# Performance work log

Hardware: AMD Instinct MI355X
Metric: run time of the kernel (lower is better)

Reference implementation:

```python
import jax, jax.numpy as jnp
import numpy as np

NT, NTR, NQ = 2048, 4096, 257  # time samples, traces, quantile knots


def cumtrapz(y, dx):
    # cumulative trapezoid along last axis, zero-prepended (preserve_dims=True)
    c = jnp.cumsum((y[..., 1:] + y[..., :-1]) * (0.5 * dx), axis=-1)
    return jnp.concatenate([jnp.zeros_like(y[..., :1]), c], axis=-1)


def trapz(y, dx):
    return (jnp.sum(y, axis=-1) - 0.5 * (y[..., 0] + y[..., -1])) * dx


def renorm(f, dx):
    # square + normalize to a pdf along time (standard W2-FWI renormalization)
    g = f * f
    return g / trapz(g, dx)[..., None]


def true_quantile(pdf, x, p, dx):
    # step-function quantile: invert clipped CDF via searchsorted per trace
    cdf = jnp.clip(cumtrapz(pdf, dx), 0.0, 1.0)  # [B, nt]
    idx = jax.vmap(lambda c: jnp.searchsorted(c, p))(cdf)  # [B, nq]
    idx = jnp.clip(idx, 0, x.shape[0] - 1)
    return x[idx]  # [B, nq]


def natural_cubic_coeffs(p, q):
    # batched natural cubic spline of q(p); knots p shared across batch
    h = p[1:] - p[:-1]                                 # [n-1]
    slope = (q[..., 1:] - q[..., :-1]) / h             # [B, n-1]
    rhs = 6.0 * (slope[..., 1:] - slope[..., :-1])     # [B, n-2]
    diag = 2.0 * (h[:-1] + h[1:])
    off = h[1:-1]
    T = jnp.diag(diag) + jnp.diag(off, 1) + jnp.diag(off, -1)  # [n-2, n-2], shared
    M_inner = jnp.linalg.solve(T, rhs[..., None])[..., 0]      # [B, n-2]
    z = jnp.zeros_like(q[..., :1])
    M = jnp.concatenate([z, M_inner, z], axis=-1)      # natural BCs: M0 = Mn = 0
    a = q[..., :-1]
    b = slope - h * (2.0 * M[..., :-1] + M[..., 1:]) / 6.0
    c = 0.5 * M[..., :-1]
    d = (M[..., 1:] - M[..., :-1]) / (6.0 * h)
    return a, b, c, d  # each [B, n-1]


def spline_eval(p, a, b, c, d, tq):
    # vectorized batched spline evaluation (replaces per-element Python loop)
    idx = jnp.clip(jnp.searchsorted(p, tq, side='left') - 1, 0, p.shape[0] - 2)
    frac = tq - p[idx]
    ga = jnp.take_along_axis(a, idx, axis=-1)
    gb = jnp.take_along_axis(b, idx, axis=-1)
    gc = jnp.take_along_axis(c, idx, axis=-1)
    gd = jnp.take_along_axis(d, idx, axis=-1)
    return ga + frac * (gb + frac * (gc + frac * gd))


def w2_forward(f, obs_data, t, p):
    dx = t[1] - t[0]
    # constructor-time part: quantile splines of observed data
    q = true_quantile(renorm(obs_data, dx), t, p, dx)   # [B, nq]
    a, b, c, d = natural_cubic_coeffs(p, q)
    # forward: CDF of synthetic, composed with observed quantile
    F = cumtrapz(renorm(f, dx), dx)                     # [B, nt]
    off_diag = spline_eval(p, a, b, c, d, F)            # [B, nt]
    diff = (t[None, :] - off_diag) ** 2
    integrated = trapz(diff * f, dx)                    # [B]
    return jnp.sum(integrated)


def setup_inputs() -> dict:
    key = jax.random.key(0)
    k1, k2 = jax.random.split(key)
    f = jax.random.normal(k1, (NTR, NT), dtype=jnp.float32)
    obs_data = jax.random.normal(k2, (NTR, NT), dtype=jnp.float32)
    t = jnp.linspace(0.0, 2.0, NT, dtype=jnp.float32)
    p = jnp.linspace(0.0, 1.0, NQ, dtype=jnp.float32)
    return {"f": f, "obs_data": obs_data, "t": t, "p": p}


def reference(f, obs_data, t, p):
    return w2_forward(f, obs_data, t, p)
```

## Files before the change

### kernel.cpp

```cpp
#include <hip/hip_runtime.h>

#define TPB 256
#define NT_ 2048
#define NQ_ 257
#define EPT 8
#define BWQ 5
#define BWS (BWQ + 2)
#define BD2 (2*BWQ + 3)
#define PQ BWQ
#define QLEN (PQ + NQ_ + BWQ + 2)
#define H_P 0.00390625f
#define RTPB 1024

struct Band { float v[BD2 * 256]; };
constexpr Band make_band() {
  Band b{};
  double L[256] = {}, winv[256] = {};
  const double H = 1.0 / 256.0;
  winv[0] = 1.0 / (4.0 * H);
  L[0] = 0.0;
  for (int i = 1; i < 255; i++) {
    L[i] = H * winv[i - 1];
    winv[i] = 1.0 / (4.0 * H - L[i] * H);
  }
  for (int i = 0; i < 255; i++) {
    double col[2 * BWS + 1] = {};
    double y[BWS + 1] = {};
    y[0] = 1.0;
    for (int m = 1; m <= BWS; m++) {
      int idx = i + m;
      y[m] = (idx <= 254) ? (-L[idx] * y[m - 1]) : 0.0;
    }
    double xn = 0.0;
    for (int m = BWS; m >= 0; m--) {
      int idx = i + m;
      double val = 0.0;
      if (idx <= 254) {
        double num = y[m] - ((idx < 254) ? H * xn : 0.0);
        val = num * winv[idx];
        xn = val;
      }
      col[m + BWS] = val;
    }
    for (int m = -1; m >= -BWS; m--) {
      int idx = i + m;
      double val = 0.0;
      if (idx >= 0) {
        val = (-H * xn) * winv[idx];
        xn = val;
      }
      col[m + BWS] = val;
    }
    for (int mm = 0; mm < BD2; mm++) {
      int n = i - BWQ + mm;
      double w = 0.0;
      if (n >= 0 && n <= 256) {
        double s0 = 0.0, s1 = 0.0, s2 = 0.0;
        int d0 = n - i, d1 = n - 1 - i, d2 = n - 2 - i;
        if (n     >= 0 && n     <= 254 && d0 >= -BWS && d0 <= BWS) s0 = col[d0 + BWS];
        if (n - 1 >= 0 && n - 1 <= 254 && d1 >= -BWS && d1 <= BWS) s1 = col[d1 + BWS];
        if (n - 2 >= 0 && n - 2 <= 254 && d2 >= -BWS && d2 <= BWS) s2 = col[d2 + BWS];
        w = 1536.0 * (s0 - 2.0 * s1 + s2);
      }
      b.v[mm * 256 + i] = (float)w;
    }
  }
  return b;
}
__device__ __constant__ Band g_band = make_band();

__device__ __forceinline__ double shfl_down_f64(double x, int off) {
  union { double d; int i[2]; } u; u.d = x;
  u.i[0] = __shfl_down(u.i[0], off, 64);
  u.i[1] = __shfl_down(u.i[1], off, 64);
  return u.d;
}

template<int CTRL, int RM, int BM, bool BC>
__device__ __forceinline__ float dppf(float x) {
  return __int_as_float(__builtin_amdgcn_update_dpp(
      0, __float_as_int(x), CTRL, RM, BM, BC));
}
template<int CTRL, int RM, int BM, bool BC>
__device__ __forceinline__ double dppd(double x) {
  union { double d; int i[2]; } u, o; u.d = x;
  o.i[0] = __builtin_amdgcn_update_dpp(0, u.i[0], CTRL, RM, BM, BC);
  o.i[1] = __builtin_amdgcn_update_dpp(0, u.i[1], CTRL, RM, BM, BC);
  return o.d;
}
__device__ __forceinline__ void iscan2(float& a, float& b) {
  a += dppf<0x111,0xF,0xF,true >(a);  b += dppf<0x111,0xF,0xF,true >(b);
  a += dppf<0x112,0xF,0xF,true >(a);  b += dppf<0x112,0xF,0xF,true >(b);
  a += dppf<0x114,0xF,0xF,true >(a);  b += dppf<0x114,0xF,0xF,true >(b);
  a += dppf<0x118,0xF,0xF,true >(a);  b += dppf<0x118,0xF,0xF,true >(b);
  a += dppf<0x142,0xa,0xF,false>(a);  b += dppf<0x142,0xa,0xF,false>(b);
  a += dppf<0x143,0xc,0xF,false>(a);  b += dppf<0x143,0xc,0xF,false>(b);
}
__device__ __forceinline__ void iscan2d(double& a, double& b) {
  a += dppd<0x111,0xF,0xF,true >(a);  b += dppd<0x111,0xF,0xF,true >(b);
  a += dppd<0x112,0xF,0xF,true >(a);  b += dppd<0x112,0xF,0xF,true >(b);
  a += dppd<0x114,0xF,0xF,true >(a);  b += dppd<0x114,0xF,0xF,true >(b);
  a += dppd<0x118,0xF,0xF,true >(a);  b += dppd<0x118,0xF,0xF,true >(b);
  a += dppd<0x142,0xa,0xF,false>(a);  b += dppd<0x142,0xa,0xF,false>(b);
  a += dppd<0x143,0xc,0xF,false>(a);  b += dppd<0x143,0xc,0xF,false>(b);
}

__global__ __launch_bounds__(TPB) void w2_main(
    const float* __restrict__ f, const float* __restrict__ obs,
    const float* __restrict__ t, double* __restrict__ row_out) {
  __shared__ float s_qA[QLEN], s_qB[QLEN];
  __shared__ float4 s_coefA[256], s_coefB[256];
  __shared__ float s_wfA[4], s_wfB[4], s_wf2A[4], s_wf2B[4];
  __shared__ double s_wdA[4], s_wdB[4];
  __shared__ double s_miscA[2], s_miscB[2];

  const int tid = threadIdx.x;
  const int lane = tid & 63;
  const int wid = tid >> 6;
  const int rowA = (int)blockIdx.x * 2;
  const int rowB = rowA + 1;
  const int base = tid * EPT;
  const int emax = (tid == TPB - 1) ? EPT - 1 : EPT;

  const double dx = (double)t[1] - (double)t[0];

  if (tid < PQ) { s_qA[tid] = 0.0f; s_qB[tid] = 0.0f; }
  if (tid >= TPB - (BWQ + 2)) {
    int o = PQ + NQ_ + tid - (TPB - (BWQ + 2));
    s_qA[o] = 0.0f; s_qB[o] = 0.0f;
  }

  float tl[EPT + 1];
  {
    const float4 a = *reinterpret_cast<const float4*>(t + base);
    const float4 b = *reinterpret_cast<const float4*>(t + base + 4);
    tl[0] = a.x; tl[1] = a.y; tl[2] = a.z; tl[3] = a.w;
    tl[4] = b.x; tl[5] = b.y; tl[6] = b.z; tl[7] = b.w;
  }
  tl[EPT] = (tid < TPB - 1) ? t[base + EPT] : 0.0f;

  float sAA[EPT], sAB[EPT];
  float epA = 0.0f, epB = 0.0f;
  {
    const float* orA = obs + (size_t)rowA * NT_;
    const float* orB = obs + (size_t)rowB * NT_;
    float ovA[EPT + 1], ovB[EPT + 1];
    {
      const float4 a0 = *reinterpret_cast<const float4*>(orA + base);
      const float4 a1 = *reinterpret_cast<const float4*>(orA + base + 4);
      const float4 b0 = *reinterpret_cast<const float4*>(orB + base);
      const float4 b1 = *reinterpret_cast<const float4*>(orB + base + 4);
      ovA[0] = a0.x; ovA[1] = a0.y; ovA[2] = a0.z; ovA[3] = a0.w;
      ovA[4] = a1.x; ovA[5] = a1.y; ovA[6] = a1.z; ovA[7] = a1.w;
      ovB[0] = b0.x; ovB[1] = b0.y; ovB[2] = b0.z; ovB[3] = b0.w;
      ovB[4] = b1.x; ovB[5] = b1.y; ovB[6] = b1.z; ovB[7] = b1.w;
    }
    ovA[EPT] = (tid < TPB - 1) ? orA[base + EPT] : 0.0f;
    ovB[EPT] = (tid < TPB - 1) ? orB[base + EPT] : 0.0f;
    for (int k = 0; k < emax; k++) {
      sAA[k] = ovA[k] * ovA[k] + ovA[k + 1] * ovA[k + 1];
      sAB[k] = ovB[k] * ovB[k] + ovB[k + 1] * ovB[k + 1];
      epA += sAA[k];
      epB += sAB[k];
    }
    if (emax < EPT) { sAA[EPT - 1] = 0.0f; sAB[EPT - 1] = 0.0f; }
  }
  float vA = epA, vB = epB;
  iscan2(vA, vB);
  float exclA = __shfl_up(vA, 1, 64);
  float exclB = __shfl_up(vB, 1, 64);
  if (lane == 0) { exclA = 0.0f; exclB = 0.0f; }
  if (lane == 63) { s_wfA[wid] = vA; s_wfB[wid] = vB; }
  __syncthreads();
  float woffA = 0.0f, totA = 0.0f, woffB = 0.0f, totB = 0.0f;
  #pragma unroll
  for (int w = 0; w < 4; w++) {
    float swA = s_wfA[w], swB = s_wfB[w];
    if (w < wid) { woffA += swA; woffB += swB; }
    totA += swA; totB += swB;
  }
  float runA = woffA + exclA, inclA = woffA + vA;
  float runB = woffB + exclB, inclB = woffB + vB;
  float invA256 = 256.0f / totA;
  float invB256 = 256.0f / totB;

  {
    float cprevS = fminf(runA * invA256, 256.0f);
    int j = (int)cprevS + 1;
    float r = runA;
    for (int k = 0; k < emax; k++) {
      float cu_uns = (k == emax - 1) ? inclA : (r + sAA[k]);
      r = cu_uns;
      float cuS = fminf(cu_uns * invA256, 256.0f);
      int jh = (int)cuS;
      float tq = tl[k + 1];
      for (; j <= jh; j++) s_qA[PQ + j] = tq;
    }
    if (tid == 0) s_qA[PQ + 0] = tl[0];
    if (tid == TPB - 1) {
      float tq = tl[EPT - 1];
      for (; j <= 256; j++) s_qA[PQ + j] = tq;
    }
  }
  {
    float cprevS = fminf(runB * invB256, 256.0f);
    int j = (int)cprevS + 1;
    float r = runB;
    for (int k = 0; k < emax; k++) {
      float cu_uns = (k == emax - 1) ? inclB : (r + sAB[k]);
      r = cu_uns;
      float cuS = fminf(cu_uns * invB256, 256.0f);
      int jh = (int)cuS;
      float tq = tl[k + 1];
      for (; j <= jh; j++) s_qB[PQ + j] = tq;
    }
    if (tid == 0) s_qB[PQ + 0] = tl[0];
    if (tid == TPB - 1) {
      float tq = tl[EPT - 1];
      for (; j <= 256; j++) s_qB[PQ + j] = tq;
    }
  }

  const float* frA = f + (size_t)rowA * NT_;
  const float* frB = f + (size_t)rowB * NT_;
  float fvA[EPT + 1], fvB[EPT + 1];
  {
    const float4 a0 = *reinterpret_cast<const float4*>(frA + base);
    const float4 a1 = *reinterpret_cast<const float4*>(frA + base + 4);
    const float4 b0 = *reinterpret_cast<const float4*>(frB + base);
    const float4 b1 = *reinterpret_cast<const float4*>(frB + base + 4);
    fvA[0] = a0.x; fvA[1] = a0.y; fvA[2] = a0.z; fvA[3] = a0.w;
    fvA[4] = a1.x; fvA[5] = a1.y; fvA[6] = a1.z; fvA[7] = a1.w;
    fvB[0] = b0.x; fvB[1] = b0.y; fvB[2] = b0.z; fvB[3] = b0.w;
    fvB[4] = b1.x; fvB[5] = b1.y; fvB[6] = b1.z; fvB[7] = b1.w;
  }
  fvA[EPT] = (tid < TPB - 1) ? frA[base + EPT] : 0.0f;
  fvB[EPT] = (tid < TPB - 1) ? frB[base + EPT] : 0.0f;

  float sBA[EPT], sBB[EPT];
  float ep2A = 0.0f, ep2B = 0.0f;
  for (int k = 0; k < emax; k++) {
    sBA[k] = fvA[k] * fvA[k] + fvA[k + 1] * fvA[k + 1];
    sBB[k] = fvB[k] * fvB[k] + fvB[k + 1] * fvB[k + 1];
    ep2A += sBA[k];
    ep2B += sBB[k];
  }
  if (emax < EPT) { sBA[EPT - 1] = 0.0f; sBB[EPT - 1] = 0.0f; }
  float v2A = ep2A, v2B = ep2B;
  iscan2(v2A, v2B);
  float excl2A = __shfl_up(v2A, 1, 64);
  float excl2B = __shfl_up(v2B, 1, 64);
  if (lane == 0) { excl2A = 0.0f; excl2B = 0.0f; }
  if (lane == 63) { s_wf2A[wid] = v2A; s_wf2B[wid] = v2B; }
  __syncthreads();

  float woff2A = 0.0f, tot2A = 0.0f, woff2B = 0.0f, tot2B = 0.0f;
  #pragma unroll
  for (int w = 0; w < 4; w++) {
    float swA = s_wf2A[w], swB = s_wf2B[w];
    if (w < wid) { woff2A += swA; woff2B += swB; }
    tot2A += swA; tot2B += swB;
  }
  float run2A = woff2A + excl2A, inv2A256 = 256.0f / tot2A;
  float run2B = woff2B + excl2B, inv2B256 = 256.0f / tot2B;

  float MregA = 0.0f, MregB = 0.0f;
  if (tid < 255) {
    #pragma unroll
    for (int mm = 0; mm < BD2; mm++) {
      float w = g_band.v[mm * 256 + tid];
      MregA += w * s_qA[tid + mm];
      MregB += w * s_qB[tid + mm];
    }
  }
  float MprevA = __shfl_up(MregA, 1, 64);
  float MprevB = __shfl_up(MregB, 1, 64);
  if (lane == 63) { s_wfA[wid] = MregA; s_wfB[wid] = MregB; }
  __syncthreads();
  if (lane == 0) {
    MprevA = (wid == 0) ? 0.0f : s_wfA[wid - 1];
    MprevB = (wid == 0) ? 0.0f : s_wfB[wid - 1];
  }

  {
    const float h = H_P;
    float q0A = s_qA[PQ + tid], q1A = s_qA[PQ + tid + 1];
    float slA = (q1A - q0A) * 256.0f;
    float bA = slA - h * (2.0f * MprevA + MregA) * (1.0f / 6.0f);
    float cA = 0.5f * MprevA;
    float dA = (MregA - MprevA) * (256.0f / 6.0f);
    s_coefA[tid] = make_float4(q0A, bA * (1.0f / 256.0f),
                               cA * (1.0f / 65536.0f), dA * (1.0f / 16777216.0f));
    float q0B = s_qB[PQ + tid], q1B = s_qB[PQ + tid + 1];
    float slB = (q1B - q0B) * 256.0f;
    float bB = slB - h * (2.0f * MprevB + MregB) * (1.0f / 6.0f);
    float cB = 0.5f * MprevB;
    float dB = (MregB - MprevB) * (256.0f / 6.0f);
    s_coefB[tid] = make_float4(q0B, bB * (1.0f / 256.0f),
                               cB * (1.0f / 65536.0f), dB * (1.0f / 16777216.0f));
  }
  __syncthreads();

  float csumA = 0.0f, csumB = 0.0f;
  {
    float r2A = run2A, r2B = run2B;
    #pragma unroll
    for (int k = 0; k < EPT; k++) {
      if (k > 0) { r2A += sBA[k - 1]; r2B += sBB[k - 1]; }
      float GA = r2A * inv2A256;
      float GB = r2B * inv2B256;
      float fiA = ceilf(GA) - 1.0f;
      float fiB = ceilf(GB) - 1.0f;
      fiA = fminf(fmaxf(fiA, 0.0f), 255.0f);
      fiB = fminf(fmaxf(fiB, 0.0f), 255.0f);
      int idxA = (int)fiA;
      int idxB = (int)fiB;
      float uA = GA - fiA;
      float uB = GB - fiB;
      float4 cfA = s_coefA[idxA];
      float4 cfB = s_coefB[idxB];
      float valA = cfA.x + uA * (cfA.y + uA * (cfA.z + uA * cfA.w));
      float valB = cfB.x + uB * (cfB.y + uB * (cfB.z + uB * cfB.w));
      float diffA = tl[k] - valA;
      float diffB = tl[k] - valB;
      float wvA = diffA * diffA * fvA[k];
      float wvB = diffB * diffB * fvB[k];
      if (tid == 0 && k == 0) { s_miscA[0] = (double)wvA; s_miscB[0] = (double)wvB; }
      if (tid == TPB - 1 && k == EPT - 1) { s_miscA[1] = (double)wvA; s_miscB[1] = (double)wvB; }
      csumA += wvA;
      csumB += wvB;
    }
  }
  double rA = (double)csumA, rB = (double)csumB;
  iscan2d(rA, rB);
  if (lane == 63) { s_wdA[wid] = rA; s_wdB[wid] = rB; }
  __syncthreads();
  if (tid == 0) {
    double totwA = s_wdA[0] + s_wdA[1] + s_wdA[2] + s_wdA[3];
    double totwB = s_wdB[0] + s_wdB[1] + s_wdB[2] + s_wdB[3];
    row_out[rowA] = (totwA - 0.5 * (s_miscA[0] + s_miscA[1])) * dx;
    row_out[rowB] = (totwB - 0.5 * (s_miscB[0] + s_miscB[1])) * dx;
  }
}

__global__ __launch_bounds__(RTPB) void w2_reduce(const double* __restrict__ row_out,
                                                  int ntr, float* __restrict__ out) {
  __shared__ double s[RTPB / 64];
  int tid = threadIdx.x, lane = tid & 63, wid = tid >> 6;
  double v = 0.0;
  for (int i = tid; i < ntr; i += RTPB) v += row_out[i];
  #pragma unroll
  for (int off = 32; off >= 1; off >>= 1) v += shfl_down_f64(v, off);
  if (lane == 0) s[wid] = v;
  __syncthreads();
  if (tid == 0) {
    double tot = 0.0;
    #pragma unroll
    for (int i = 0; i < RTPB / 64; i++) tot += s[i];
    out[0] = (float)tot;
  }
}

extern "C" void kernel_launch(void* const* d_in, const int* in_sizes, int n_in,
                              void* d_out, int out_size, void* d_ws, size_t ws_size,
                              hipStream_t stream) {
  const float* f   = (const float*)d_in[0];
  const float* obs = (const float*)d_in[1];
  const float* t   = (const float*)d_in[2];
  int nt = in_sizes[2];
  int ntr = in_sizes[0] / nt;

  double* rows = (double*)d_ws;

  hipLaunchKernelGGL(w2_main, dim3(ntr / 2), dim3(TPB), 0, stream,
                     f, obs, t, rows);
  hipLaunchKernelGGL(w2_reduce, dim3(1), dim3(RTPB), 0, stream,
                     rows, ntr, (float*)d_out);
}
```

Before: 35.80 us.

## Double block size, halve per-thread work, split spline coefficient build across halves

Raises the block to 512 threads with 4 elements per thread, so each thread does less serial work and there are more waves per row pair. The two rows' spline coefficient computation is now split across the two 256-thread halves, and boundary Mprev values are recomputed locally instead of exchanged through a shared-memory barrier. The f loads are hoisted next to the obs loads so more memory traffic is in flight early. The final reduction uses a float wave scan plus double accumulation across waves, dropping the double DPP scan. This costs precision in the per-wave partial sums, more waves to synchronise per block, and duplicated band arithmetic at wave boundaries.

```diff
diff --git a/kernel.cpp b/kernel.cpp
--- a/kernel.cpp
+++ b/kernel.cpp
@@ -1,9 +1,10 @@
 #include <hip/hip_runtime.h>
 
-#define TPB 256
+#define TPB 512
+#define NW (TPB/64)
 #define NT_ 2048
 #define NQ_ 257
-#define EPT 8
+#define EPT 4
 #define BWQ 5
 #define BWS (BWQ + 2)
 #define BD2 (2*BWQ + 3)
@@ -81,13 +82,6 @@
   return __int_as_float(__builtin_amdgcn_update_dpp(
       0, __float_as_int(x), CTRL, RM, BM, BC));
 }
-template<int CTRL, int RM, int BM, bool BC>
-__device__ __forceinline__ double dppd(double x) {
-  union { double d; int i[2]; } u, o; u.d = x;
-  o.i[0] = __builtin_amdgcn_update_dpp(0, u.i[0], CTRL, RM, BM, BC);
-  o.i[1] = __builtin_amdgcn_update_dpp(0, u.i[1], CTRL, RM, BM, BC);
-  return o.d;
-}
 __device__ __forceinline__ void iscan2(float& a, float& b) {
   a += dppf<0x111,0xF,0xF,true >(a);  b += dppf<0x111,0xF,0xF,true >(b);
   a += dppf<0x112,0xF,0xF,true >(a);  b += dppf<0x112,0xF,0xF,true >(b);
@@ -96,23 +90,14 @@
   a += dppf<0x142,0xa,0xF,false>(a);  b += dppf<0x142,0xa,0xF,false>(b);
   a += dppf<0x143,0xc,0xF,false>(a);  b += dppf<0x143,0xc,0xF,false>(b);
 }
-__device__ __forceinline__ void iscan2d(double& a, double& b) {
-  a += dppd<0x111,0xF,0xF,true >(a);  b += dppd<0x111,0xF,0xF,true >(b);
-  a += dppd<0x112,0xF,0xF,true >(a);  b += dppd<0x112,0xF,0xF,true >(b);
-  a += dppd<0x114,0xF,0xF,true >(a);  b += dppd<0x114,0xF,0xF,true >(b);
-  a += dppd<0x118,0xF,0xF,true >(a);  b += dppd<0x118,0xF,0xF,true >(b);
-  a += dppd<0x142,0xa,0xF,false>(a);  b += dppd<0x142,0xa,0xF,false>(b);
-  a += dppd<0x143,0xc,0xF,false>(a);  b += dppd<0x143,0xc,0xF,false>(b);
-}
 
 __global__ __launch_bounds__(TPB) void w2_main(
     const float* __restrict__ f, const float* __restrict__ obs,
     const float* __restrict__ t, double* __restrict__ row_out) {
   __shared__ float s_qA[QLEN], s_qB[QLEN];
   __shared__ float4 s_coefA[256], s_coefB[256];
-  __shared__ float s_wfA[4], s_wfB[4], s_wf2A[4], s_wf2B[4];
-  __shared__ double s_wdA[4], s_wdB[4];
-  __shared__ double s_miscA[2], s_miscB[2];
+  __shared__ float s_wfA[NW], s_wfB[NW], s_wf2A[NW], s_wf2B[NW];
+  __shared__ float s_ends[4];
 
   const int tid = threadIdx.x;
   const int lane = tid & 63;
@@ -133,38 +118,40 @@
   float tl[EPT + 1];
   {
     const float4 a = *reinterpret_cast<const float4*>(t + base);
-    const float4 b = *reinterpret_cast<const float4*>(t + base + 4);
     tl[0] = a.x; tl[1] = a.y; tl[2] = a.z; tl[3] = a.w;
-    tl[4] = b.x; tl[5] = b.y; tl[6] = b.z; tl[7] = b.w;
   }
   tl[EPT] = (tid < TPB - 1) ? t[base + EPT] : 0.0f;
+
+  const float* orA = obs + (size_t)rowA * NT_;
+  const float* orB = obs + (size_t)rowB * NT_;
+  const float* frA = f + (size_t)rowA * NT_;
+  const float* frB = f + (size_t)rowB * NT_;
+  float ovA[EPT + 1], ovB[EPT + 1], fvA[EPT + 1], fvB[EPT + 1];
+  {
+    const float4 a0 = *reinterpret_cast<const float4*>(orA + base);
+    const float4 b0 = *reinterpret_cast<const float4*>(orB + base);
+    const float4 c0 = *reinterpret_cast<const float4*>(frA + base);
+    const float4 d0 = *reinterpret_cast<const float4*>(frB + base);
+    ovA[0] = a0.x; ovA[1] = a0.y; ovA[2] = a0.z; ovA[3] = a0.w;
+    ovB[0] = b0.x; ovB[1] = b0.y; ovB[2] = b0.z; ovB[3] = b0.w;
+    fvA[0] = c0.x; fvA[1] = c0.y; fvA[2] = c0.z; fvA[3] = c0.w;
+    fvB[0] = d0.x; fvB[1] = d0.y; fvB[2] = d0.z; fvB[3] = d0.w;
+  }
+  const bool notlast = (tid < TPB - 1);
+  ovA[EPT] = notlast ? orA[base + EPT] : 0.0f;
+  ovB[EPT] = notlast ? orB[base + EPT] : 0.0f;
+  fvA[EPT] = notlast ? frA[base + EPT] : 0.0f;
+  fvB[EPT] = notlast ? frB[base + EPT] : 0.0f;
 
   float sAA[EPT], sAB[EPT];
   float epA = 0.0f, epB = 0.0f;
-  {
-    const float* orA = obs + (size_t)rowA * NT_;
-    const float* orB = obs + (size_t)rowB * NT_;
-    float ovA[EPT + 1], ovB[EPT + 1];
-    {
-      const float4 a0 = *reinterpret_cast<const float4*>(orA + base);
-      const float4 a1 = *reinterpret_cast<const float4*>(orA + base + 4);
-      const float4 b0 = *reinterpret_cast<const float4*>(orB + base);
-      const float4 b1 = *reinterpret_cast<const float4*>(orB + base + 4);
-      ovA[0] = a0.x; ovA[1] = a0.y; ovA[2] = a0.z; ovA[3] = a0.w;
-      ovA[4] = a1.x; ovA[5] = a1.y; ovA[6] = a1.z; ovA[7] = a1.w;
-      ovB[0] = b0.x; ovB[1] = b0.y; ovB[2] = b0.z; ovB[3] = b0.w;
-      ovB[4] = b1.x; ovB[5] = b1.y; ovB[6] = b1.z; ovB[7] = b1.w;
-    }
-    ovA[EPT] = (tid < TPB - 1) ? orA[base + EPT] : 0.0f;
-    ovB[EPT] = (tid < TPB - 1) ? orB[base + EPT] : 0.0f;
-    for (int k = 0; k < emax; k++) {
-      sAA[k] = ovA[k] * ovA[k] + ovA[k + 1] * ovA[k + 1];
-      sAB[k] = ovB[k] * ovB[k] + ovB[k + 1] * ovB[k + 1];
-      epA += sAA[k];
-      epB += sAB[k];
-    }
-    if (emax < EPT) { sAA[EPT - 1] = 0.0f; sAB[EPT - 1] = 0.0f; }
-  }
+  for (int k = 0; k < emax; k++) {
+    sAA[k] = ovA[k] * ovA[k] + ovA[k + 1] * ovA[k + 1];
+    sAB[k] = ovB[k] * ovB[k] + ovB[k + 1] * ovB[k + 1];
+    epA += sAA[k];
+    epB += sAB[k];
+  }
+  if (emax < EPT) { sAA[EPT - 1] = 0.0f; sAB[EPT - 1] = 0.0f; }
   float vA = epA, vB = epB;
   iscan2(vA, vB);
   float exclA = __shfl_up(vA, 1, 64);
@@ -174,7 +161,7 @@
   __syncthreads();
   float woffA = 0.0f, totA = 0.0f, woffB = 0.0f, totB = 0.0f;
   #pragma unroll
-  for (int w = 0; w < 4; w++) {
+  for (int w = 0; w < NW; w++) {
     float swA = s_wfA[w], swB = s_wfB[w];
     if (w < wid) { woffA += swA; woffB += swB; }
     totA += swA; totB += swB;
@@ -221,22 +208,6 @@
     }
   }
 
-  const float* frA = f + (size_t)rowA * NT_;
-  const float* frB = f + (size_t)rowB * NT_;
-  float fvA[EPT + 1], fvB[EPT + 1];
-  {
-    const float4 a0 = *reinterpret_cast<const float4*>(frA + base);
-    const float4 a1 = *reinterpret_cast<const float4*>(frA + base + 4);
-    const float4 b0 = *reinterpret_cast<const float4*>(frB + base);
-    const float4 b1 = *reinterpret_cast<const float4*>(frB + base + 4);
-    fvA[0] = a0.x; fvA[1] = a0.y; fvA[2] = a0.z; fvA[3] = a0.w;
-    fvA[4] = a1.x; fvA[5] = a1.y; fvA[6] = a1.z; fvA[7] = a1.w;
-    fvB[0] = b0.x; fvB[1] = b0.y; fvB[2] = b0.z; fvB[3] = b0.w;
-    fvB[4] = b1.x; fvB[5] = b1.y; fvB[6] = b1.z; fvB[7] = b1.w;
-  }
-  fvA[EPT] = (tid < TPB - 1) ? frA[base + EPT] : 0.0f;
-  fvB[EPT] = (tid < TPB - 1) ? frB[base + EPT] : 0.0f;
-
   float sBA[EPT], sBB[EPT];
   float ep2A = 0.0f, ep2B = 0.0f;
   for (int k = 0; k < emax; k++) {
@@ -256,7 +227,7 @@
 
   float woff2A = 0.0f, tot2A = 0.0f, woff2B = 0.0f, tot2B = 0.0f;
   #pragma unroll
-  for (int w = 0; w < 4; w++) {
+  for (int w = 0; w < NW; w++) {
     float swA = s_wf2A[w], swB = s_wf2B[w];
     if (w < wid) { woff2A += swA; woff2B += swB; }
     tot2A += swA; tot2B += swB;
@@ -264,44 +235,37 @@
   float run2A = woff2A + excl2A, inv2A256 = 256.0f / tot2A;
   float run2B = woff2B + excl2B, inv2B256 = 256.0f / tot2B;
 
-  float MregA = 0.0f, MregB = 0.0f;
-  if (tid < 255) {
-    #pragma unroll
-    for (int mm = 0; mm < BD2; mm++) {
-      float w = g_band.v[mm * 256 + tid];
-      MregA += w * s_qA[tid + mm];
-      MregB += w * s_qB[tid + mm];
-    }
-  }
-  float MprevA = __shfl_up(MregA, 1, 64);
-  float MprevB = __shfl_up(MregB, 1, 64);
-  if (lane == 63) { s_wfA[wid] = MregA; s_wfB[wid] = MregB; }
-  __syncthreads();
-  if (lane == 0) {
-    MprevA = (wid == 0) ? 0.0f : s_wfA[wid - 1];
-    MprevB = (wid == 0) ? 0.0f : s_wfB[wid - 1];
-  }
-
-  {
-    const float h = H_P;
-    float q0A = s_qA[PQ + tid], q1A = s_qA[PQ + tid + 1];
-    float slA = (q1A - q0A) * 256.0f;
-    float bA = slA - h * (2.0f * MprevA + MregA) * (1.0f / 6.0f);
-    float cA = 0.5f * MprevA;
-    float dA = (MregA - MprevA) * (256.0f / 6.0f);
-    s_coefA[tid] = make_float4(q0A, bA * (1.0f / 256.0f),
-                               cA * (1.0f / 65536.0f), dA * (1.0f / 16777216.0f));
-    float q0B = s_qB[PQ + tid], q1B = s_qB[PQ + tid + 1];
-    float slB = (q1B - q0B) * 256.0f;
-    float bB = slB - h * (2.0f * MprevB + MregB) * (1.0f / 6.0f);
-    float cB = 0.5f * MprevB;
-    float dB = (MregB - MprevB) * (256.0f / 6.0f);
-    s_coefB[tid] = make_float4(q0B, bB * (1.0f / 256.0f),
-                               cB * (1.0f / 65536.0f), dB * (1.0f / 16777216.0f));
+  {
+    const int half = tid >> 8;
+    const int hi = tid & 255;
+    const float* qrow = half ? s_qB : s_qA;
+    float4* coefh = half ? s_coefB : s_coefA;
+    float Mreg = 0.0f;
+    if (hi < 255) {
+      #pragma unroll
+      for (int mm = 0; mm < BD2; mm++)
+        Mreg += g_band.v[mm * 256 + hi] * qrow[hi + mm];
+    }
+    float Mprev = __shfl_up(Mreg, 1, 64);
+    if ((hi & 63) == 0) {
+      Mprev = 0.0f;
+      if (hi > 0) {
+        #pragma unroll
+        for (int mm = 0; mm < BD2; mm++)
+          Mprev += g_band.v[mm * 256 + (hi - 1)] * qrow[hi - 1 + mm];
+      }
+    }
+    float q0 = qrow[PQ + hi], q1 = qrow[PQ + hi + 1];
+    float sl = (q1 - q0) * 256.0f;
+    float bb = sl - H_P * (2.0f * Mprev + Mreg) * (1.0f / 6.0f);
+    coefh[hi] = make_float4(q0, bb * (1.0f / 256.0f),
+                            Mprev * (1.0f / 131072.0f),
+                            (Mreg - Mprev) * (1.0f / 393216.0f));
   }
   __syncthreads();
 
   float csumA = 0.0f, csumB = 0.0f;
+  float wvA = 0.0f, wvB = 0.0f;
   {
     float r2A = run2A, r2B = run2B;
     #pragma unroll
@@ -323,23 +287,32 @@
       float valB = cfB.x + uB * (cfB.y + uB * (cfB.z + uB * cfB.w));
       float diffA = tl[k] - valA;
       float diffB = tl[k] - valB;
-      float wvA = diffA * diffA * fvA[k];
-      float wvB = diffB * diffB * fvB[k];
-      if (tid == 0 && k == 0) { s_miscA[0] = (double)wvA; s_miscB[0] = (double)wvB; }
-      if (tid == TPB - 1 && k == EPT - 1) { s_miscA[1] = (double)wvA; s_miscB[1] = (double)wvB; }
+      wvA = diffA * diffA * fvA[k];
+      wvB = diffB * diffB * fvB[k];
       csumA += wvA;
       csumB += wvB;
     }
   }
-  double rA = (double)csumA, rB = (double)csumB;
-  iscan2d(rA, rB);
-  if (lane == 63) { s_wdA[wid] = rA; s_wdB[wid] = rB; }
-  __syncthreads();
   if (tid == 0) {
-    double totwA = s_wdA[0] + s_wdA[1] + s_wdA[2] + s_wdA[3];
-    double totwB = s_wdB[0] + s_wdB[1] + s_wdB[2] + s_wdB[3];
-    row_out[rowA] = (totwA - 0.5 * (s_miscA[0] + s_miscA[1])) * dx;
-    row_out[rowB] = (totwB - 0.5 * (s_miscB[0] + s_miscB[1])) * dx;
+    float dA = tl[0] - s_coefA[0].x;
+    float dB = tl[0] - s_coefB[0].x;
+    s_ends[0] = dA * dA * fvA[0];
+    s_ends[2] = dB * dB * fvB[0];
+  }
+  if (tid == TPB - 1) { s_ends[1] = wvA; s_ends[3] = wvB; }
+
+  iscan2(csumA, csumB);
+  if (lane == 63) { s_wfA[wid] = csumA; s_wfB[wid] = csumB; }
+  __syncthreads();
+  if (tid == 0) {
+    double totwA = 0.0, totwB = 0.0;
+    #pragma unroll
+    for (int w = 0; w < NW; w++) {
+      totwA += (double)s_wfA[w];
+      totwB += (double)s_wfB[w];
+    }
+    row_out[rowA] = (totwA - 0.5 * ((double)s_ends[0] + (double)s_ends[1])) * dx;
+    row_out[rowB] = (totwB - 0.5 * ((double)s_ends[2] + (double)s_ends[3])) * dx;
   }
 }
 
```

Result: no change. 35.89 us (+0.2%).
